# Kernel optimization log

Hardware: AMD Instinct MI355X
Metric: run time of the kernel (lower is better)

Reference implementation:

```python
import jax, jax.numpy as jnp
import numpy as np

LATENT_SIZE = 1024
WORD_SIZE = 64
NB_WORD = 8192
COMMIT_VQ = 2.5
BATCH = 2048


def setup_inputs() -> dict:
    key = jax.random.key(0)
    k1, k2, k3 = jax.random.split(key, 3)
    z_mean = jax.random.normal(k1, (BATCH, LATENT_SIZE), dtype=jnp.float32)
    z_log_var = jax.random.normal(k2, (BATCH, LATENT_SIZE), dtype=jnp.float32)
    # Embedding initialized uniform(-1/nb_word, 1/nb_word) in the torch module;
    # use normal here for a numerically non-degenerate correctness baseline.
    emb_weight = jax.random.normal(k3, (NB_WORD, WORD_SIZE), dtype=jnp.float32)
    return {"z_mean": z_mean, "z_log_var": z_log_var, "emb_weight": emb_weight}


def reference(z_mean, z_log_var, emb_weight):
    sg = jax.lax.stop_gradient
    input_shape = z_mean.shape
    # (B * latent/word, word)
    z = z_mean.reshape(-1, LATENT_SIZE // WORD_SIZE, WORD_SIZE)
    z_flat = z.reshape(-1, WORD_SIZE)
    # squared euclidean distances: (N, nb_word)
    distances = (
        jnp.sum(z_flat ** 2, axis=1, keepdims=True)
        + jnp.sum(emb_weight ** 2, axis=1)
        - 2.0 * jnp.einsum("bd,nd->bn", z_flat, emb_weight)
    )
    min_idx = jnp.argmin(distances, axis=1)  # (N,)
    z_q = emb_weight[min_idx].reshape(z.shape)  # gather codebook vectors
    loss = (
        jnp.mean((sg(z_q) - z) ** 2)
        + COMMIT_VQ * jnp.mean((z_q - sg(z)) ** 2)
    )
    z_q_st = z + sg(z_q - z)  # straight-through estimator
    return z_q_st.reshape(input_shape), loss
```

## Files before the change

kernel.cpp:

```cpp
#include <hip/hip_runtime.h>
#include <math.h>

#define LATENT   1024
#define WORD     64
#define NB_WORD  8192
#define BATCH    2048
#define NROWS    (BATCH * LATENT / WORD)
#define NELEM    (BATCH * LATENT)

#define NCHUNK   8
#define CWCHUNK  (NB_WORD / NCHUNK)
#define TPC      (CWCHUNK / 16)
#define NTILE    (NB_WORD / 16)
#define PKTS     (NTILE * 6 * 64)

typedef __attribute__((ext_vector_type(8))) __bf16 bf16x8;
typedef __attribute__((ext_vector_type(4))) float  f32x4;

__global__ __launch_bounds__(256) void vq_e2_kernel(
    const float* __restrict__ emb, float* __restrict__ e2) {
    int m = blockIdx.x * 256 + threadIdx.x;
    if (m >= NB_WORD) return;
    const float4* ep = reinterpret_cast<const float4*>(emb + (size_t)m * WORD);
    float s0 = 0.f, s1 = 0.f, s2 = 0.f, s3 = 0.f;
#pragma unroll
    for (int i = 0; i < 16; ++i) {
        float4 v = ep[i];
        s0 = fmaf(v.x, v.x, s0);
        s1 = fmaf(v.y, v.y, s1);
        s2 = fmaf(v.z, v.z, s2);
        s3 = fmaf(v.w, v.w, s3);
    }
    e2[m] = (s0 + s1) + (s2 + s3);
}

__global__ __launch_bounds__(256) void vq_epack_kernel(
    const float* __restrict__ emb, bf16x8* __restrict__ epack) {
    int p = blockIdx.x * 256 + threadIdx.x;
    int lane = p & 63;
    int q    = p >> 6;
    int Ks   = q & 1;
    int r    = q >> 1;
    int spl  = r % 3;
    int tile = r / 3;
    int cw = tile * 16 + (lane & 15);
    int k0 = Ks * 32 + (lane >> 4) * 8;
    const float4* s4 = reinterpret_cast<const float4*>(emb + (size_t)cw * WORD + k0);
    float4 a = s4[0], b = s4[1];
    float tv[8] = {a.x, a.y, a.z, a.w, b.x, b.y, b.z, b.w};
    bf16x8 o;
#pragma unroll
    for (int e = 0; e < 8; ++e) {
        float v = tv[e];
        __bf16 h  = (__bf16)v;
        float r1  = v - (float)h;
        __bf16 m  = (__bf16)r1;
        float r2  = r1 - (float)m;
        __bf16 lo = (__bf16)r2;
        o[e] = (spl == 0) ? h : ((spl == 1) ? m : lo);
    }
    epack[p] = o;
}

__device__ __forceinline__ void gload_lds16(const char* g, char* l) {
    __builtin_amdgcn_global_load_lds(
        (const __attribute__((address_space(1))) void*)g,
        (__attribute__((address_space(3))) void*)l, 16, 0, 0);
}

__global__ __launch_bounds__(256)
__attribute__((amdgpu_waves_per_eu(4, 8)))
void vq_argmin_kernel(
    const float* __restrict__ z, const bf16x8* __restrict__ epack,
    const float* __restrict__ e2, unsigned long long* __restrict__ best) {

    {
        int ph = blockIdx.x & 3;
        if (ph == 1) __builtin_amdgcn_s_sleep(2);
        else if (ph == 2) __builtin_amdgcn_s_sleep(4);
        else if (ph == 3) __builtin_amdgcn_s_sleep(6);
    }

    __shared__ __align__(16) char le[2 * 6144];

    const int tid   = threadIdx.x;
    const int lane  = tid & 63;
    const int wband = tid >> 6;
    const int l15   = lane & 15;
    const int l4    = lane >> 4;
    const int rowbase   = blockIdx.x * 128 + wband * 32;
    const int tile0     = blockIdx.y * TPC;
    const int chunkbase = blockIdx.y * CWCHUNK;
    const float* e2g    = e2 + chunkbase;
    const int off       = (blockIdx.x & 15) * 4;

    bf16x8 A[2][2][3];
    const float4* zf4 = reinterpret_cast<const float4*>(z);
#pragma unroll
    for (int mt = 0; mt < 2; ++mt) {
        int row = rowbase + mt * 16 + l15;
#pragma unroll
        for (int Ks = 0; Ks < 2; ++Ks) {
            float4 v0 = zf4[(size_t)row * 16 + Ks * 8 + l4 * 2];
            float4 v1 = zf4[(size_t)row * 16 + Ks * 8 + l4 * 2 + 1];
            float tv[8] = {v0.x, v0.y, v0.z, v0.w, v1.x, v1.y, v1.z, v1.w};
#pragma unroll
            for (int e = 0; e < 8; ++e) {
                float v = tv[e];
                __bf16 h  = (__bf16)v;
                float r1  = v - (float)h;
                __bf16 m  = (__bf16)r1;
                float r2  = r1 - (float)m;
                __bf16 lo = (__bf16)r2;
                A[mt][Ks][0][e] = h;
                A[mt][Ks][1][e] = m;
                A[mt][Ks][2][e] = lo;
            }
        }
    }

    {
        const char* src = (const char*)epack + (size_t)(tile0 + off) * 6144;
        gload_lds16(src + wband * 1024 + lane * 16, le + wband * 1024);
        if (wband < 2)
            gload_lds16(src + (4 + wband) * 1024 + lane * 16,
                        le + (4 + wband) * 1024);
    }
    float e2next = e2g[off * 16 + l15];

    float bestd[8] = {INFINITY, INFINITY, INFINITY, INFINITY,
                      INFINITY, INFINITY, INFINITY, INFINITY};
    int   bt[8]    = {0, 0, 0, 0, 0, 0, 0, 0};

    for (int tt = 0; tt < TPC; ++tt) {
        const int buf = tt & 1;
        const int t   = (tt + off) & (TPC - 1);

        asm volatile("s_waitcnt vmcnt(0)" ::: "memory");
        __builtin_amdgcn_sched_barrier(0);
        __builtin_amdgcn_s_barrier();

        const float e2v = e2next;

        {
            const int tn = (tt + 1 + off) & (TPC - 1);
            const char* src = (const char*)epack + (size_t)(tile0 + tn) * 6144;
            char* dst = le + (buf ^ 1) * 6144;
            gload_lds16(src + wband * 1024 + lane * 16, dst + wband * 1024);
            if (wband < 2)
                gload_lds16(src + (4 + wband) * 1024 + lane * 16,
                            dst + (4 + wband) * 1024);
            e2next = e2g[tn * 16 + l15];
        }

        f32x4 acc0 = {0.f, 0.f, 0.f, 0.f};
        f32x4 acc1 = {0.f, 0.f, 0.f, 0.f};
        __builtin_amdgcn_s_setprio(1);
#pragma unroll
        for (int Ks = 0; Ks < 2; ++Ks) {
            const char* bbase = le + buf * 6144 + (size_t)Ks * 1024 + lane * 16;
            bf16x8 Bh = *reinterpret_cast<const bf16x8*>(bbase);
            bf16x8 Bm = *reinterpret_cast<const bf16x8*>(bbase + 2048);
            bf16x8 Bl = *reinterpret_cast<const bf16x8*>(bbase + 4096);
            acc0 = __builtin_amdgcn_mfma_f32_16x16x32_bf16(A[0][Ks][0], Bh, acc0, 0, 0, 0);
            acc1 = __builtin_amdgcn_mfma_f32_16x16x32_bf16(A[1][Ks][0], Bh, acc1, 0, 0, 0);
            acc0 = __builtin_amdgcn_mfma_f32_16x16x32_bf16(A[0][Ks][1], Bh, acc0, 0, 0, 0);
            acc1 = __builtin_amdgcn_mfma_f32_16x16x32_bf16(A[1][Ks][1], Bh, acc1, 0, 0, 0);
            acc0 = __builtin_amdgcn_mfma_f32_16x16x32_bf16(A[0][Ks][2], Bh, acc0, 0, 0, 0);
            acc1 = __builtin_amdgcn_mfma_f32_16x16x32_bf16(A[1][Ks][2], Bh, acc1, 0, 0, 0);
            acc0 = __builtin_amdgcn_mfma_f32_16x16x32_bf16(A[0][Ks][0], Bm, acc0, 0, 0, 0);
            acc1 = __builtin_amdgcn_mfma_f32_16x16x32_bf16(A[1][Ks][0], Bm, acc1, 0, 0, 0);
            acc0 = __builtin_amdgcn_mfma_f32_16x16x32_bf16(A[0][Ks][1], Bm, acc0, 0, 0, 0);
            acc1 = __builtin_amdgcn_mfma_f32_16x16x32_bf16(A[1][Ks][1], Bm, acc1, 0, 0, 0);
            acc0 = __builtin_amdgcn_mfma_f32_16x16x32_bf16(A[0][Ks][0], Bl, acc0, 0, 0, 0);
            acc1 = __builtin_amdgcn_mfma_f32_16x16x32_bf16(A[1][Ks][0], Bl, acc1, 0, 0, 0);
        }
        __builtin_amdgcn_s_setprio(0);

#pragma unroll
        for (int v = 0; v < 4; ++v) {
            float d0 = fmaf(-2.0f, acc0[v], e2v);
            if (d0 < bestd[v])     { bestd[v]     = d0; bt[v]     = t; }
            float d1 = fmaf(-2.0f, acc1[v], e2v);
            if (d1 < bestd[4 + v]) { bestd[4 + v] = d1; bt[4 + v] = t; }
        }
    }

#pragma unroll
    for (int mt = 0; mt < 2; ++mt) {
#pragma unroll
        for (int v = 0; v < 4; ++v) {
            float bd = bestd[mt * 4 + v];
            int   cw = chunkbase + bt[mt * 4 + v] * 16 + l15;
            unsigned db = __float_as_uint(bd);
            db = (db & 0x80000000u) ? ~db : (db | 0x80000000u);
            unsigned long long key =
                ((unsigned long long)db << 32) | (unsigned)cw;
#pragma unroll
            for (int off2 = 1; off2 < 16; off2 <<= 1) {
                unsigned long long o = __shfl_xor(key, off2);
                key = (o < key) ? o : key;
            }
            if (l15 == 0)
                atomicMin(&best[rowbase + mt * 16 + l4 * 4 + v], key);
        }
    }
}

__global__ __launch_bounds__(256) void vq_out_kernel(
    const float* __restrict__ z, const float* __restrict__ emb,
    const unsigned long long* __restrict__ best,
    float* __restrict__ out, float* __restrict__ lsum) {
    const int base = (blockIdx.x * 256 + threadIdx.x) * 8;
    const int row  = base >> 6;
    const int m    = (int)(best[row] & 0xFFFFFFFFull);

    const float4* zp = reinterpret_cast<const float4*>(z + base);
    const float4* qp = reinterpret_cast<const float4*>(emb + (size_t)m * WORD + (base & 63));
    float4* op = reinterpret_cast<float4*>(out + base);

    float s = 0.f;
#pragma unroll
    for (int i = 0; i < 2; ++i) {
        float4 zv = zp[i];
        float4 qv = qp[i];
        float dx = qv.x - zv.x, dy = qv.y - zv.y, dz = qv.z - zv.z, dw = qv.w - zv.w;
        float4 ov;
        ov.x = zv.x + dx; ov.y = zv.y + dy; ov.z = zv.z + dz; ov.w = zv.w + dw;
        op[i] = ov;
        s += dx*dx + dy*dy + dz*dz + dw*dw;
    }

#pragma unroll
    for (int off = 32; off > 0; off >>= 1) s += __shfl_down(s, off);
    __shared__ float wsum[4];
    int lane = threadIdx.x & 63, wid = threadIdx.x >> 6;
    if (lane == 0) wsum[wid] = s;
    __syncthreads();
    if (threadIdx.x == 0)
        atomicAdd(lsum, (wsum[0] + wsum[1]) + (wsum[2] + wsum[3]));
}

__global__ void vq_loss_kernel(const float* __restrict__ lsum,
                               float* __restrict__ loss_out) {
    float mean = lsum[0] * (1.0f / (float)NELEM);
    loss_out[0] = mean + 2.5f * mean;
}

extern "C" void kernel_launch(void* const* d_in, const int* in_sizes, int n_in,
                              void* d_out, int out_size, void* d_ws, size_t ws_size,
                              hipStream_t stream) {
    const float* z   = (const float*)d_in[0];
    const float* emb = (const float*)d_in[2];
    float* out = (float*)d_out;

    bf16x8* epack = (bf16x8*)d_ws;
    float*  e2    = (float*)((char*)d_ws + (size_t)PKTS * 16);
    unsigned long long* best =
        (unsigned long long*)((char*)e2 + NB_WORD * sizeof(float));
    float* lsum = (float*)((char*)best + NROWS * sizeof(unsigned long long));

    hipMemsetAsync(best, 0xFF, NROWS * sizeof(unsigned long long), stream);
    hipMemsetAsync(lsum, 0, sizeof(float), stream);

    vq_e2_kernel<<<NB_WORD / 256, 256, 0, stream>>>(emb, e2);
    vq_epack_kernel<<<PKTS / 256, 256, 0, stream>>>(emb, epack);
    vq_argmin_kernel<<<dim3(NROWS / 128, NCHUNK), 256, 0, stream>>>(
        z, epack, e2, best);
    vq_out_kernel<<<NELEM / (256 * 8), 256, 0, stream>>>(z, emb, best, out, lsum);
    vq_loss_kernel<<<1, 1, 0, stream>>>(lsum, out + NELEM);
}
```

Baseline: 194.6 us.

## Fuse codebook prep kernels and software-pipeline argmin epilogue behind MFMAs

Merges the e2 norm kernel and the bf16 split-packing kernel into one prep kernel, so each thread reads its codeword once and writes all three split packets plus the norm. This removes one launch and a redundant read of the codebook. In the argmin loop, all six B fragments are loaded from LDS up front, and the distance compare for the previous tile is deferred so it overlaps the current tile's MFMA chain. The cost is extra live registers for the previous accumulators, which could reduce occupancy.

```diff
diff --git a/kernel.cpp b/kernel.cpp
--- a/kernel.cpp
+++ b/kernel.cpp
@@ -17,49 +17,42 @@
 typedef __attribute__((ext_vector_type(8))) __bf16 bf16x8;
 typedef __attribute__((ext_vector_type(4))) float  f32x4;
 
-__global__ __launch_bounds__(256) void vq_e2_kernel(
-    const float* __restrict__ emb, float* __restrict__ e2) {
+__global__ __launch_bounds__(256) void vq_prep_kernel(
+    const float* __restrict__ emb, float* __restrict__ e2,
+    bf16x8* __restrict__ epack) {
     int m = blockIdx.x * 256 + threadIdx.x;
-    if (m >= NB_WORD) return;
-    const float4* ep = reinterpret_cast<const float4*>(emb + (size_t)m * WORD);
+    int tile = m >> 4, l15 = m & 15;
     float s0 = 0.f, s1 = 0.f, s2 = 0.f, s3 = 0.f;
 #pragma unroll
-    for (int i = 0; i < 16; ++i) {
-        float4 v = ep[i];
-        s0 = fmaf(v.x, v.x, s0);
-        s1 = fmaf(v.y, v.y, s1);
-        s2 = fmaf(v.z, v.z, s2);
-        s3 = fmaf(v.w, v.w, s3);
+    for (int Ks = 0; Ks < 2; ++Ks) {
+#pragma unroll
+        for (int q = 0; q < 4; ++q) {
+            const float4* s4 = reinterpret_cast<const float4*>(
+                emb + (size_t)m * WORD + Ks * 32 + q * 8);
+            float4 a = s4[0], b = s4[1];
+            float tv[8] = {a.x, a.y, a.z, a.w, b.x, b.y, b.z, b.w};
+            bf16x8 oh, om, ol;
+#pragma unroll
+            for (int e = 0; e < 8; ++e) {
+                float v = tv[e];
+                if ((e & 3) == 0) s0 = fmaf(v, v, s0);
+                else if ((e & 3) == 1) s1 = fmaf(v, v, s1);
+                else if ((e & 3) == 2) s2 = fmaf(v, v, s2);
+                else s3 = fmaf(v, v, s3);
+                __bf16 h  = (__bf16)v;
+                float r1  = v - (float)h;
+                __bf16 mm = (__bf16)r1;
+                float r2  = r1 - (float)mm;
+                __bf16 lo = (__bf16)r2;
+                oh[e] = h; om[e] = mm; ol[e] = lo;
+            }
+            size_t base = ((size_t)tile * 6) * 64 + q * 16 + l15;
+            epack[base + (size_t)(0 * 2 + Ks) * 64] = oh;
+            epack[base + (size_t)(1 * 2 + Ks) * 64] = om;
+            epack[base + (size_t)(2 * 2 + Ks) * 64] = ol;
+        }
     }
     e2[m] = (s0 + s1) + (s2 + s3);
-}
-
-__global__ __launch_bounds__(256) void vq_epack_kernel(
-    const float* __restrict__ emb, bf16x8* __restrict__ epack) {
-    int p = blockIdx.x * 256 + threadIdx.x;
-    int lane = p & 63;
-    int q    = p >> 6;
-    int Ks   = q & 1;
-    int r    = q >> 1;
-    int spl  = r % 3;
-    int tile = r / 3;
-    int cw = tile * 16 + (lane & 15);
-    int k0 = Ks * 32 + (lane >> 4) * 8;
-    const float4* s4 = reinterpret_cast<const float4*>(emb + (size_t)cw * WORD + k0);
-    float4 a = s4[0], b = s4[1];
-    float tv[8] = {a.x, a.y, a.z, a.w, b.x, b.y, b.z, b.w};
-    bf16x8 o;
-#pragma unroll
-    for (int e = 0; e < 8; ++e) {
-        float v = tv[e];
-        __bf16 h  = (__bf16)v;
-        float r1  = v - (float)h;
-        __bf16 m  = (__bf16)r1;
-        float r2  = r1 - (float)m;
-        __bf16 lo = (__bf16)r2;
-        o[e] = (spl == 0) ? h : ((spl == 1) ? m : lo);
-    }
-    epack[p] = o;
 }
 
 __device__ __forceinline__ void gload_lds16(const char* g, char* l) {
@@ -132,6 +125,11 @@
                       INFINITY, INFINITY, INFINITY, INFINITY};
     int   bt[8]    = {0, 0, 0, 0, 0, 0, 0, 0};
 
+    f32x4 pacc0 = {0.f, 0.f, 0.f, 0.f};
+    f32x4 pacc1 = {0.f, 0.f, 0.f, 0.f};
+    float e2prev = INFINITY;
+    int   tprev  = 0;
+
     for (int tt = 0; tt < TPC; ++tt) {
         const int buf = tt & 1;
         const int t   = (tt + off) & (TPC - 1);
@@ -153,37 +151,60 @@
             e2next = e2g[tn * 16 + l15];
         }
 
+        const char* b0 = le + buf * 6144 + lane * 16;
+        bf16x8 Bh0 = *reinterpret_cast<const bf16x8*>(b0);
+        bf16x8 Bm0 = *reinterpret_cast<const bf16x8*>(b0 + 2048);
+        bf16x8 Bl0 = *reinterpret_cast<const bf16x8*>(b0 + 4096);
+        bf16x8 Bh1 = *reinterpret_cast<const bf16x8*>(b0 + 1024);
+        bf16x8 Bm1 = *reinterpret_cast<const bf16x8*>(b0 + 3072);
+        bf16x8 Bl1 = *reinterpret_cast<const bf16x8*>(b0 + 5120);
+
+#pragma unroll
+        for (int v = 0; v < 4; ++v) {
+            float d0 = fmaf(-2.0f, pacc0[v], e2prev);
+            if (d0 < bestd[v])     { bestd[v]     = d0; bt[v]     = tprev; }
+            float d1 = fmaf(-2.0f, pacc1[v], e2prev);
+            if (d1 < bestd[4 + v]) { bestd[4 + v] = d1; bt[4 + v] = tprev; }
+        }
+
         f32x4 acc0 = {0.f, 0.f, 0.f, 0.f};
         f32x4 acc1 = {0.f, 0.f, 0.f, 0.f};
         __builtin_amdgcn_s_setprio(1);
-#pragma unroll
-        for (int Ks = 0; Ks < 2; ++Ks) {
-            const char* bbase = le + buf * 6144 + (size_t)Ks * 1024 + lane * 16;
-            bf16x8 Bh = *reinterpret_cast<const bf16x8*>(bbase);
-            bf16x8 Bm = *reinterpret_cast<const bf16x8*>(bbase + 2048);
-            bf16x8 Bl = *reinterpret_cast<const bf16x8*>(bbase + 4096);
-            acc0 = __builtin_amdgcn_mfma_f32_16x16x32_bf16(A[0][Ks][0], Bh, acc0, 0, 0, 0);
-            acc1 = __builtin_amdgcn_mfma_f32_16x16x32_bf16(A[1][Ks][0], Bh, acc1, 0, 0, 0);
-            acc0 = __builtin_amdgcn_mfma_f32_16x16x32_bf16(A[0][Ks][1], Bh, acc0, 0, 0, 0);
-            acc1 = __builtin_amdgcn_mfma_f32_16x16x32_bf16(A[1][Ks][1], Bh, acc1, 0, 0, 0);
-            acc0 = __builtin_amdgcn_mfma_f32_16x16x32_bf16(A[0][Ks][2], Bh, acc0, 0, 0, 0);
-            acc1 = __builtin_amdgcn_mfma_f32_16x16x32_bf16(A[1][Ks][2], Bh, acc1, 0, 0, 0);
-            acc0 = __builtin_amdgcn_mfma_f32_16x16x32_bf16(A[0][Ks][0], Bm, acc0, 0, 0, 0);
-            acc1 = __builtin_amdgcn_mfma_f32_16x16x32_bf16(A[1][Ks][0], Bm, acc1, 0, 0, 0);
-            acc0 = __builtin_amdgcn_mfma_f32_16x16x32_bf16(A[0][Ks][1], Bm, acc0, 0, 0, 0);
-            acc1 = __builtin_amdgcn_mfma_f32_16x16x32_bf16(A[1][Ks][1], Bm, acc1, 0, 0, 0);
-            acc0 = __builtin_amdgcn_mfma_f32_16x16x32_bf16(A[0][Ks][0], Bl, acc0, 0, 0, 0);
-            acc1 = __builtin_amdgcn_mfma_f32_16x16x32_bf16(A[1][Ks][0], Bl, acc1, 0, 0, 0);
-        }
+        acc0 = __builtin_amdgcn_mfma_f32_16x16x32_bf16(A[0][0][0], Bh0, acc0, 0, 0, 0);
+        acc1 = __builtin_amdgcn_mfma_f32_16x16x32_bf16(A[1][0][0], Bh0, acc1, 0, 0, 0);
+        acc0 = __builtin_amdgcn_mfma_f32_16x16x32_bf16(A[0][0][1], Bh0, acc0, 0, 0, 0);
+        acc1 = __builtin_amdgcn_mfma_f32_16x16x32_bf16(A[1][0][1], Bh0, acc1, 0, 0, 0);
+        acc0 = __builtin_amdgcn_mfma_f32_16x16x32_bf16(A[0][0][2], Bh0, acc0, 0, 0, 0);
+        acc1 = __builtin_amdgcn_mfma_f32_16x16x32_bf16(A[1][0][2], Bh0, acc1, 0, 0, 0);
+        acc0 = __builtin_amdgcn_mfma_f32_16x16x32_bf16(A[0][0][0], Bm0, acc0, 0, 0, 0);
+        acc1 = __builtin_amdgcn_mfma_f32_16x16x32_bf16(A[1][0][0], Bm0, acc1, 0, 0, 0);
+        acc0 = __builtin_amdgcn_mfma_f32_16x16x32_bf16(A[0][0][1], Bm0, acc0, 0, 0, 0);
+        acc1 = __builtin_amdgcn_mfma_f32_16x16x32_bf16(A[1][0][1], Bm0, acc1, 0, 0, 0);
+        acc0 = __builtin_amdgcn_mfma_f32_16x16x32_bf16(A[0][0][0], Bl0, acc0, 0, 0, 0);
+        acc1 = __builtin_amdgcn_mfma_f32_16x16x32_bf16(A[1][0][0], Bl0, acc1, 0, 0, 0);
+        acc0 = __builtin_amdgcn_mfma_f32_16x16x32_bf16(A[0][1][0], Bh1, acc0, 0, 0, 0);
+        acc1 = __builtin_amdgcn_mfma_f32_16x16x32_bf16(A[1][1][0], Bh1, acc1, 0, 0, 0);
+        acc0 = __builtin_amdgcn_mfma_f32_16x16x32_bf16(A[0][1][1], Bh1, acc0, 0, 0, 0);
+        acc1 = __builtin_amdgcn_mfma_f32_16x16x32_bf16(A[1][1][1], Bh1, acc1, 0, 0, 0);
+        acc0 = __builtin_amdgcn_mfma_f32_16x16x32_bf16(A[0][1][2], Bh1, acc0, 0, 0, 0);
+        acc1 = __builtin_amdgcn_mfma_f32_16x16x32_bf16(A[1][1][2], Bh1, acc1, 0, 0, 0);
+        acc0 = __builtin_amdgcn_mfma_f32_16x16x32_bf16(A[0][1][0], Bm1, acc0, 0, 0, 0);
+        acc1 = __builtin_amdgcn_mfma_f32_16x16x32_bf16(A[1][1][0], Bm1, acc1, 0, 0, 0);
+        acc0 = __builtin_amdgcn_mfma_f32_16x16x32_bf16(A[0][1][1], Bm1, acc0, 0, 0, 0);
+        acc1 = __builtin_amdgcn_mfma_f32_16x16x32_bf16(A[1][1][1], Bm1, acc1, 0, 0, 0);
+        acc0 = __builtin_amdgcn_mfma_f32_16x16x32_bf16(A[0][1][0], Bl1, acc0, 0, 0, 0);
+        acc1 = __builtin_amdgcn_mfma_f32_16x16x32_bf16(A[1][1][0], Bl1, acc1, 0, 0, 0);
         __builtin_amdgcn_s_setprio(0);
 
-#pragma unroll
-        for (int v = 0; v < 4; ++v) {
-            float d0 = fmaf(-2.0f, acc0[v], e2v);
-            if (d0 < bestd[v])     { bestd[v]     = d0; bt[v]     = t; }
-            float d1 = fmaf(-2.0f, acc1[v], e2v);
-            if (d1 < bestd[4 + v]) { bestd[4 + v] = d1; bt[4 + v] = t; }
-        }
+        pacc0 = acc0; pacc1 = acc1; e2prev = e2v; tprev = t;
+    }
+
+#pragma unroll
+    for (int v = 0; v < 4; ++v) {
+        float d0 = fmaf(-2.0f, pacc0[v], e2prev);
+        if (d0 < bestd[v])     { bestd[v]     = d0; bt[v]     = tprev; }
+        float d1 = fmaf(-2.0f, pacc1[v], e2prev);
+        if (d1 < bestd[4 + v]) { bestd[4 + v] = d1; bt[4 + v] = tprev; }
     }
 
 #pragma unroll
@@ -263,8 +284,7 @@
     hipMemsetAsync(best, 0xFF, NROWS * sizeof(unsigned long long), stream);
     hipMemsetAsync(lsum, 0, sizeof(float), stream);
 
-    vq_e2_kernel<<<NB_WORD / 256, 256, 0, stream>>>(emb, e2);
-    vq_epack_kernel<<<PKTS / 256, 256, 0, stream>>>(emb, epack);
+    vq_prep_kernel<<<NB_WORD / 256, 256, 0, stream>>>(emb, e2, epack);
     vq_argmin_kernel<<<dim3(NROWS / 128, NCHUNK), 256, 0, stream>>>(
         z, epack, e2, best);
     vq_out_kernel<<<NELEM / (256 * 8), 256, 0, stream>>>(z, emb, best, out, lsum);
```

New measurement: 189.6 us. 1.03x faster.
